# Performance work log

Hardware: AMD Instinct MI355X
Metric: run time of the kernel (lower is better)

The kernel has to match this reference:

```python
import jax, jax.numpy as jnp
import numpy as np

DIM = 512
NUM_HEADS = 16
D_HEAD = DIM // NUM_HEADS
B, S = 4, 1024


def _relative_shift(pos_score):
    # pos_score: [B, H, S1, S2] -> Transformer-XL relative shift
    b, h, s1, s2 = pos_score.shape
    padded = jnp.pad(pos_score, ((0, 0), (0, 0), (0, 0), (1, 0)))  # [B,H,S1,S2+1]
    padded = padded.reshape(b, h, s2 + 1, s1)
    return padded[:, :, 1:].reshape(b, h, s1, s2)


def setup_inputs() -> dict:
    key = jax.random.key(0)
    ks = jax.random.split(key, 16)
    f32 = jnp.float32
    scale = 0.02
    inp = {
        "query": jax.random.normal(ks[0], (B, S, DIM), f32),
        "key": jax.random.normal(ks[1], (B, S, DIM), f32),
        "value": jax.random.normal(ks[2], (B, S, DIM), f32),
        "pos_embedding": jax.random.normal(ks[3], (B, S, DIM), f32),
        "Wq": jax.random.normal(ks[4], (DIM, DIM), f32) * scale,
        "bq": jnp.zeros((DIM,), f32),
        "Wk": jax.random.normal(ks[5], (DIM, DIM), f32) * scale,
        "bk": jnp.zeros((DIM,), f32),
        "Wv": jax.random.normal(ks[6], (DIM, DIM), f32) * scale,
        "bv": jnp.zeros((DIM,), f32),
        "Wp": jax.random.normal(ks[7], (DIM, DIM), f32) * scale,  # pos_proj, no bias
        "u_bias": jax.random.normal(ks[8], (NUM_HEADS, D_HEAD), f32) * scale,
        "v_bias": jax.random.normal(ks[9], (NUM_HEADS, D_HEAD), f32) * scale,
        "Wo": jax.random.normal(ks[10], (DIM, DIM), f32) * scale,
        "bo": jnp.zeros((DIM,), f32),
    }
    return inp


def reference(query, key, value, pos_embedding, Wq, bq, Wk, bk, Wv, bv, Wp,
              u_bias, v_bias, Wo, bo):
    b = query.shape[0]
    # projections (torch Linear: x @ W.T + b), split heads -> [B, S, H, Dh]
    q = (query @ Wq.T + bq).reshape(b, -1, NUM_HEADS, D_HEAD)
    k = (key @ Wk.T + bk).reshape(b, -1, NUM_HEADS, D_HEAD)
    v = (value @ Wv.T + bv).reshape(b, -1, NUM_HEADS, D_HEAD)
    p = (pos_embedding @ Wp.T).reshape(b, -1, NUM_HEADS, D_HEAD)

    # content score: (q + u) @ k^T  -> [B, H, Sq, Sk]
    content_score = jnp.einsum('bqhd,bkhd->bhqk', q + u_bias, k)
    # position score: (q + v) @ pos^T, then relative shift
    pos_score = jnp.einsum('bqhd,bkhd->bhqk', q + v_bias, p)
    pos_score = _relative_shift(pos_score)

    score = (content_score + pos_score) / np.sqrt(D_HEAD).astype(np.float32)
    attn = jax.nn.softmax(score, axis=-1)  # dropout_p = 0.0 -> identity

    context = jnp.einsum('bhqk,bkhd->bqhd', attn, v).reshape(b, -1, DIM)
    return context @ Wo.T + bo
```

## Files before the change

kernel.cpp:

```cpp
#include <hip/hip_runtime.h>
#include <hip/hip_bf16.h>
#include <math.h>


typedef float f32x4 __attribute__((ext_vector_type(4)));
typedef __bf16 bf16x8 __attribute__((ext_vector_type(8)));
typedef __bf16 bf16x2 __attribute__((ext_vector_type(2)));

#define MFMA16(a, b, c) __builtin_amdgcn_mfma_f32_16x16x32_bf16((a), (b), (c), 0, 0, 0)

constexpr int Bb  = 4;
constexpr int S   = 1024;
constexpr int H   = 16;
constexpr int Dh  = 32;
constexpr int DIM = 512;
constexpr float SCALEL2E = 0.25501818637084186f;
constexpr int ZROWS = 3 * S + 16;

constexpr size_t XN = (size_t)Bb * S * DIM;
constexpr size_t WN = (size_t)DIM * DIM;

__device__ inline bf16x8 cvt8(const float* __restrict__ p) {
  f32x4 a = *(const f32x4*)p;
  f32x4 b = *(const f32x4*)(p + 4);
  bf16x8 r;
  r[0] = (__bf16)a[0]; r[1] = (__bf16)a[1]; r[2] = (__bf16)a[2]; r[3] = (__bf16)a[3];
  r[4] = (__bf16)b[0]; r[5] = (__bf16)b[1]; r[6] = (__bf16)b[2]; r[7] = (__bf16)b[3];
  return r;
}

__device__ inline float fexp2(float x) {
  float r;
  asm("v_exp_f32 %0, %1" : "=v"(r) : "v"(x));
  return r;
}

__device__ inline void gload_lds16(const __bf16* g, __bf16* l) {
  __builtin_amdgcn_global_load_lds(
      (const __attribute__((address_space(1))) unsigned int*)g,
      (__attribute__((address_space(3))) unsigned int*)l, 16, 0, 0);
}

__global__ __launch_bounds__(256) void conv_kernel(
    const float* __restrict__ q, const float* __restrict__ k,
    const float* __restrict__ v, const float* __restrict__ p,
    const float* __restrict__ wq, const float* __restrict__ wk,
    const float* __restrict__ wv, const float* __restrict__ wp,
    const float* __restrict__ wo,
    __bf16* __restrict__ xb, __bf16* __restrict__ wb,
    __bf16* __restrict__ phZ)
{
  const int y = blockIdx.y;
  if (y == 9) {
    const int e8 = blockIdx.x * 256 + threadIdx.x;
    if (e8 < 64 * 136 * 4) {
      const int rowIdx = e8 >> 2, chunk = e8 & 3;
      const int bh = rowIdx / 136;
      const int rl = rowIdx - bh * 136;
      const int row = (rl < 72) ? (960 + rl) : (2040 + (rl - 72));
      bf16x8 zz = {};
      *(bf16x8*)(phZ + ((size_t)bh * ZROWS + row) * Dh + chunk * 8) = zz;
    }
    return;
  }
  const float* src;
  size_t n;
  __bf16* dst;
  if (y < 4) {
    src = (y == 0) ? q : (y == 1) ? k : (y == 2) ? v : p;
    n = XN;
    dst = xb + (size_t)y * XN;
  } else {
    const int w = y - 4;
    src = (w == 0) ? wq : (w == 1) ? wk : (w == 2) ? wv : (w == 3) ? wp : wo;
    n = WN;
    dst = wb + (size_t)w * WN;
  }
  const size_t i = ((size_t)blockIdx.x * 256 + threadIdx.x) * 8;
  if (i >= n) return;
  *(bf16x8*)(dst + i) = cvt8(src + i);
}

template <int MODE>
__global__ __launch_bounds__(256) void gemm_kernel(
    const __bf16* __restrict__ xb, const __bf16* __restrict__ wb,
    const __bf16* __restrict__ ctxp,
    const float* __restrict__ bq, const float* __restrict__ bk,
    const float* __restrict__ bv, const float* __restrict__ bo,
    const float* __restrict__ ub, const float* __restrict__ vb,
    __bf16* __restrict__ qu, __bf16* __restrict__ qv,
    __bf16* __restrict__ kk, __bf16* __restrict__ vt,
    __bf16* __restrict__ phZ,
    float* __restrict__ outp)
{
  constexpr int MR = (MODE == 0) ? 4 : 2;
  constexpr int BM = MR * 32;
  __shared__ __align__(16) __bf16 smem[BM * 64 + 128 * 64];
  __bf16* As = smem;
  __bf16* Bs = smem + BM * 64;
  __bf16* trans = smem;

  const int bid = blockIdx.x;
  const int u = bid >> 3;
  const int by = u & 3;
  const int idx = (bid & 7) + 8 * (u >> 2);
  int bx, z;
  if (MODE == 0) { bx = idx & 31; z = idx >> 5; }
  else           { bx = idx;      z = 4; }

  const __bf16* Ag = (z < 4) ? (xb + (size_t)z * XN) : ctxp;
  const __bf16* Bg = wb + (size_t)z * WN;

  const int tid = threadIdx.x;
  const int wid = tid >> 6;
  const int ln = tid & 63;
  const int lm = ln & 15, lg = ln >> 4;
  const int wr = wid >> 1, wc = wid & 1;
  const int brow = bx * BM;
  const int bcol = by * 128;

  const int srow = ln >> 3;
  const int sc   = ln & 7;

  f32x4 acc[MR][4] = {};

  for (int kt = 0; kt < DIM / 64; ++kt) {
    const int k0 = kt * 64;
#pragma unroll
    for (int i = 0; i < MR; ++i) {
      const int rb = wid * (MR * 8) + i * 8;
      const int r = rb + srow;
      const int cg = sc ^ (r & 7);
      gload_lds16(Ag + (size_t)(brow + r) * DIM + k0 + cg * 8, &As[rb * 64]);
    }
#pragma unroll
    for (int i = 0; i < 4; ++i) {
      const int rb = wid * 32 + i * 8;
      const int r = rb + srow;
      const int cg = sc ^ (r & 7);
      gload_lds16(Bg + (size_t)(bcol + r) * DIM + k0 + cg * 8, &Bs[rb * 64]);
    }
    __syncthreads();

#pragma unroll
    for (int ks = 0; ks < 2; ++ks) {
      bf16x8 a[MR], b[4];
#pragma unroll
      for (int m = 0; m < MR; ++m) {
        const int row = wr * (MR * 16) + m * 16 + lm;
        const int cc = (ks * 4 + lg) ^ (row & 7);
        a[m] = *(const bf16x8*)&As[row * 64 + cc * 8];
      }
#pragma unroll
      for (int n = 0; n < 4; ++n) {
        const int row = wc * 64 + n * 16 + lm;
        const int cc = (ks * 4 + lg) ^ (row & 7);
        b[n] = *(const bf16x8*)&Bs[row * 64 + cc * 8];
      }
#pragma unroll
      for (int m = 0; m < MR; ++m)
#pragma unroll
        for (int n = 0; n < 4; ++n)
          acc[m][n] = MFMA16(a[m], b[n], acc[m][n]);
    }
    __syncthreads();
  }

  if (MODE == 0 && z == 2) {
    const int b = brow >> 10;
    const int sbase = brow & (S - 1);
#pragma unroll
    for (int n = 0; n < 4; ++n) {
      const int dl = wc * 64 + n * 16 + lm;
      const float bias = bv[bcol + dl];
#pragma unroll
      for (int mp = 0; mp < 2; ++mp) {
#pragma unroll
        for (int r = 0; r < 4; ++r) {
          const int p = wr * 64 + mp * 32 + 2 * (lg * 4 + r);
          bf16x2 pk;
          pk[0] = (__bf16)(acc[2 * mp][n][r] + bias);
          pk[1] = (__bf16)(acc[2 * mp + 1][n][r] + bias);
          const int base = dl * 128 + (((p >> 3) ^ (dl & 15)) * 8) + (p & 7);
          *(bf16x2*)(trans + base) = pk;
        }
      }
    }
    __syncthreads();
#pragma unroll
    for (int j = 0; j < 4; ++j) {
      const int dl = (tid >> 3) + j * 32;
      const int d = dl & 31, hl = dl >> 5;
      const int cp = (tid & 7) * 2;
      bf16x8 v0 = *(const bf16x8*)(trans + dl * 128 + ((cp ^ (dl & 15)) * 8));
      bf16x8 v1 = *(const bf16x8*)(trans + dl * 128 + (((cp + 1) ^ (dl & 15)) * 8));
      const int bh2 = b * H + (bcol >> 5) + hl;
      __bf16* dst = vt + ((size_t)bh2 * Dh + d) * S + sbase + cp * 8;
      *(bf16x8*)dst = v0;
      *(bf16x8*)(dst + 8) = v1;
    }
    return;
  }

#pragma unroll
  for (int n = 0; n < 4; ++n) {
    const int o = bcol + wc * 64 + n * 16 + lm;
    float bias = 0.f, ubv = 0.f, vbv = 0.f;
    if (z == 0) { bias = bq[o]; ubv = ub[o]; vbv = vb[o]; }
    else if (z == 1) bias = bk[o];
    else if (z == 4) bias = bo[o];
    const int h = o >> 5, d = o & 31;
#pragma unroll
    for (int m = 0; m < MR; ++m) {
#pragma unroll
      for (int r = 0; r < 4; ++r) {
        const int M = brow + wr * (MR * 16) + m * 16 + lg * 4 + r;
        const float val = acc[m][n][r];
        if (z == 4) {
          outp[(size_t)M * DIM + o] = val + bias;
          continue;
        }
        const int b = M >> 10, s = M & (S - 1);
        const int bh = b * H + h;
        if (z == 0) {
          const size_t idx2 = ((size_t)bh * S + s) * Dh + d;
          qu[idx2] = (__bf16)((val + bias + ubv) * SCALEL2E);
          qv[idx2] = (__bf16)((val + bias + vbv) * SCALEL2E);
        } else if (z == 1) {
          kk[((size_t)bh * S + s) * Dh + d] = (__bf16)(val + bias);
        } else {
          phZ[((size_t)bh * ZROWS + (S + 1 + s)) * Dh + d] = (__bf16)val;
        }
      }
    }
  }
}

__global__ __launch_bounds__(256, 4) void attn_kernel(
    const __bf16* __restrict__ qu, const __bf16* __restrict__ qv,
    const __bf16* __restrict__ kk, const __bf16* __restrict__ vt,
    const __bf16* __restrict__ phZ,
    __bf16* __restrict__ ctx)
{
  __shared__ __align__(16) __bf16 kv_lds[4][2][1024];
  __shared__ __align__(16) __bf16 at_all[4][2][16 * 40];

  const int tid = threadIdx.x;
  const int wid = tid >> 6;
  const int l = tid & 63;
  const int lm = l & 15, lg = l >> 4;

  const int bid = blockIdx.x;
  const int bh = (bid & 7) + 8 * ((bid >> 3) & 7);
  const int q0 = (bid >> 6) * 64 + wid * 16;
  const int h = bh & (H - 1), b = bh >> 4;

  const __bf16* qub = qu + (size_t)bh * S * Dh;
  const __bf16* qvb = qv + (size_t)bh * S * Dh;
  const __bf16* kb  = kk + (size_t)bh * S * Dh;
  const __bf16* vtb = vt + (size_t)bh * Dh * S;
  const __bf16* pZb = phZ + (size_t)bh * ZROWS * Dh;
  const __bf16* pAb = pZb + (size_t)(S + 1) * Dh;

  const bf16x8 au  = *(const bf16x8*)(qub + (size_t)(q0 + lm) * Dh + lg * 8);
  const bf16x8 avA = *(const bf16x8*)(qvb + (size_t)(q0 + lm) * Dh + lg * 8);
  const bf16x8 avB = *(const bf16x8*)(qvb + (size_t)(q0 + 1 + lm) * Dh + lg * 8);

  int  slr[4];
  bool prd[4];
#pragma unroll
  for (int r = 0; r < 4; ++r) {
    const int qr = lg * 4 + r;
    slr[r] = (l & 48) | ((lm - qr + 15) & 15);
    prd[r] = (lm <= qr);
  }

  bf16x8 ones8;
#pragma unroll
  for (int i = 0; i < 8; ++i) ones8[i] = (__bf16)1.0f;

  f32x4 cta = {0.f,0.f,0.f,0.f}, ctb = {0.f,0.f,0.f,0.f};
  f32x4 ls  = {0.f,0.f,0.f,0.f};
  const f32x4 zero4 = {0.f,0.f,0.f,0.f};

  const int srow = l >> 2;
  const int scg  = ((l & 3) ^ (srow & 3)) * 8;
  auto stage = [&](int kt, int buf) {
    const __bf16* src;
    if (wid == 0)      src = kb  + (size_t)(kt + srow) * Dh + scg;
    else if (wid == 1) src = kb  + (size_t)(kt + 16 + srow) * Dh + scg;
    else if (wid == 2) src = vtb + (size_t)srow * S + kt + scg;
    else               src = vtb + (size_t)(16 + srow) * S + kt + scg;
    gload_lds16(src, &kv_lds[buf][wid >> 1][(wid & 1) * 512]);
  };

  const int cc = (lg ^ (lm & 3)) * 8;

  auto zwin = [&](int kt, bf16x8& z0, bf16x8& z1, bf16x8& z2, bool& uB) {
    const int ktc = (kt < S) ? kt : (S - 32);
    uB = (ktc > q0 - 31);
    const int mb = ktc - q0 + (S - 16);
    const __bf16* zb = uB ? pZb : pAb;
    z0 = *(const bf16x8*)(zb + (size_t)(mb + lm) * Dh + lg * 8);
    z1 = *(const bf16x8*)(zb + (size_t)(mb + 16 + lm) * Dh + lg * 8);
    z2 = *(const bf16x8*)(zb + (size_t)(mb + 32 + lm) * Dh + lg * 8);
  };

  auto half = [&](int kt, int tb, __bf16* at,
                  bf16x8 z0, bf16x8 z1, bf16x8 z2, bool uB) {
    const __bf16* Ks = kv_lds[tb][0];
    const __bf16* Vs = kv_lds[tb][1];
    bf16x8 kf0 = *(const bf16x8*)(Ks + lm * 32 + cc);
    bf16x8 kf1 = *(const bf16x8*)(Ks + (lm + 16) * 32 + cc);
    __builtin_amdgcn_s_setprio(1);
    f32x4 c0 = MFMA16(au, kf0, zero4);
    f32x4 c1 = MFMA16(au, kf1, zero4);
    const bf16x8 av = uB ? avB : avA;
    f32x4 pt0 = MFMA16(av, z0, zero4);
    f32x4 pt1 = MFMA16(av, z1, zero4);
    f32x4 pt2 = MFMA16(av, z2, zero4);
    __builtin_amdgcn_s_setprio(0);
    if (uB && (kt < q0 + 16)) {
      const int mb = kt - q0 + (S - 16);
      bf16x8 y0 = *(const bf16x8*)(pAb + (size_t)(mb + lm) * Dh + lg * 8);
      bf16x8 y1 = *(const bf16x8*)(pAb + (size_t)(mb + 16 + lm) * Dh + lg * 8);
      bf16x8 y2 = *(const bf16x8*)(pAb + (size_t)(mb + 32 + lm) * Dh + lg * 8);
      pt0 = MFMA16(avA, y0, pt0);
      pt1 = MFMA16(avA, y1, pt1);
      pt2 = MFMA16(avA, y2, pt2);
    }

#pragma unroll
    for (int r = 0; r < 4; ++r) {
      const float v0 = __shfl(pt0[r], slr[r], 64);
      const float v1 = __shfl(pt1[r], slr[r], 64);
      const float v2 = __shfl(pt2[r], slr[r], 64);
      const float s0 = c0[r] + (prd[r] ? v0 : v1);
      const float s1 = c1[r] + (prd[r] ? v1 : v2);
      bf16x2 pp;
      pp[0] = (__bf16)fexp2(s0);
      pp[1] = (__bf16)fexp2(s1);
      *(bf16x2*)(at + (lg * 4 + r) * 40 + 2 * lm) = pp;
    }

    bf16x8 af  = *(const bf16x8*)(at + lm * 40 + lg * 8);
    bf16x8 vf0 = *(const bf16x8*)(Vs + lm * 32 + cc);
    bf16x8 vf1 = *(const bf16x8*)(Vs + (lm + 16) * 32 + cc);
    __builtin_amdgcn_s_setprio(1);
    cta = MFMA16(af, vf0, cta);
    ctb = MFMA16(af, vf1, ctb);
    ls  = MFMA16(af, ones8, ls);
    __builtin_amdgcn_s_setprio(0);
  };

  __bf16* at0 = at_all[wid][0];
  __bf16* at1 = at_all[wid][1];

  bf16x8 zA0, zA1, zA2, zB0, zB1, zB2;
  bool uA, uB;
  zwin(0, zA0, zA1, zA2, uA);
  stage(0, 0);
  stage(32, 1);
  asm volatile("s_waitcnt vmcnt(0)" ::: "memory");
  __builtin_amdgcn_s_barrier();

  for (int kt = 0; kt < S; kt += 64) {
    const int t = kt >> 5;
    stage((kt + 64 < S) ? kt + 64 : kt, (t + 2) & 3);
    stage((kt + 96 < S) ? kt + 96 : kt, (t + 3) & 3);
    zwin(kt + 32, zB0, zB1, zB2, uB);
    half(kt, t & 3, at0, zA0, zA1, zA2, uA);
    zwin(kt + 64, zA0, zA1, zA2, uA);
    half(kt + 32, (t + 1) & 3, at1, zB0, zB1, zB2, uB);

    asm volatile("s_waitcnt vmcnt(3)" ::: "memory");
    __builtin_amdgcn_s_barrier();
  }

#pragma unroll
  for (int r = 0; r < 4; ++r) {
    const int s0 = q0 + lg * 4 + r;
    const float inv = 1.f / ls[r];
    __bf16* cp = ctx + ((size_t)b * S + s0) * DIM + h * Dh;
    cp[lm]      = (__bf16)(cta[r] * inv);
    cp[16 + lm] = (__bf16)(ctb[r] * inv);
  }
}

extern "C" void kernel_launch(void* const* d_in, const int* in_sizes, int n_in,
                              void* d_out, int out_size, void* d_ws, size_t ws_size,
                              hipStream_t stream) {
  const float* query = (const float*)d_in[0];
  const float* key   = (const float*)d_in[1];
  const float* value = (const float*)d_in[2];
  const float* pos   = (const float*)d_in[3];
  const float* Wq = (const float*)d_in[4];
  const float* bq = (const float*)d_in[5];
  const float* Wk = (const float*)d_in[6];
  const float* bk = (const float*)d_in[7];
  const float* Wv = (const float*)d_in[8];
  const float* bv = (const float*)d_in[9];
  const float* Wp = (const float*)d_in[10];
  const float* ub = (const float*)d_in[11];
  const float* vb = (const float*)d_in[12];
  const float* Wo = (const float*)d_in[13];
  const float* bo = (const float*)d_in[14];
  float* out = (float*)d_out;

  char* ws = (char*)d_ws;
  const size_t MB = 1ull << 20;
  __bf16* xb  = (__bf16*)(ws + 0 * MB);
  __bf16* wb  = (__bf16*)(ws + 16 * MB);
  __bf16* qu  = (__bf16*)(ws + 19 * MB);
  __bf16* qv  = (__bf16*)(ws + 23 * MB);
  __bf16* kk  = (__bf16*)(ws + 27 * MB);
  __bf16* vt  = (__bf16*)(ws + 31 * MB);
  __bf16* phZ = (__bf16*)(ws + 35 * MB);
  __bf16* ctx = (__bf16*)(ws + 48 * MB);

  conv_kernel<<<dim3(1024, 10), dim3(256), 0, stream>>>(
      query, key, value, pos, Wq, Wk, Wv, Wp, Wo, xb, wb, phZ);

  gemm_kernel<0><<<dim3(512), dim3(256), 0, stream>>>(
      xb, wb, ctx, bq, bk, bv, bo, ub, vb,
      qu, qv, kk, vt, phZ, out);

  attn_kernel<<<dim3(1024), dim3(256), 0, stream>>>(
      qu, qv, kk, vt, phZ, ctx);

  gemm_kernel<1><<<dim3(256), dim3(256), 0, stream>>>(
      xb, wb, ctx, bq, bk, bv, bo, ub, vb,
      qu, qv, kk, vt, phZ, out);
}
```

Baseline: 84.21 us.

## Reuse overlapping positional windows across tiles and change LDS swizzle pattern

The positional window loads for consecutive 32-key tiles overlap by 16 rows, so the third chunk of one window is reused as the first chunk of the next when both come from the same buffer. This removes one global/L2 load per half-tile in the common case. The K/V LDS swizzle is also changed to XOR with a different row-bit group, on both the staging writes and the fragment reads, to alter the bank conflict pattern. There is a risk that the extra branches and the register dependencies across halves lengthen live ranges or serialize loads.

```diff
diff --git a/kernel.cpp b/kernel.cpp
--- a/kernel.cpp
+++ b/kernel.cpp
@@ -284,7 +284,7 @@
   const f32x4 zero4 = {0.f,0.f,0.f,0.f};
 
   const int srow = l >> 2;
-  const int scg  = ((l & 3) ^ (srow & 3)) * 8;
+  const int scg  = ((l & 3) ^ ((l >> 3) & 3)) * 8;
   auto stage = [&](int kt, int buf) {
     const __bf16* src;
     if (wid == 0)      src = kb  + (size_t)(kt + srow) * Dh + scg;
@@ -294,20 +294,16 @@
     gload_lds16(src, &kv_lds[buf][wid >> 1][(wid & 1) * 512]);
   };
 
-  const int cc = (lg ^ (lm & 3)) * 8;
-
-  auto zwin = [&](int kt, bf16x8& z0, bf16x8& z1, bf16x8& z2, bool& uB) {
-    const int ktc = (kt < S) ? kt : (S - 32);
-    uB = (ktc > q0 - 31);
+  const int cc = (lg ^ ((lm >> 1) & 3)) * 8;
+
+  auto zld = [&](int ktc, int off, bool uB_) -> bf16x8 {
     const int mb = ktc - q0 + (S - 16);
-    const __bf16* zb = uB ? pZb : pAb;
-    z0 = *(const bf16x8*)(zb + (size_t)(mb + lm) * Dh + lg * 8);
-    z1 = *(const bf16x8*)(zb + (size_t)(mb + 16 + lm) * Dh + lg * 8);
-    z2 = *(const bf16x8*)(zb + (size_t)(mb + 32 + lm) * Dh + lg * 8);
+    const __bf16* zb = uB_ ? pZb : pAb;
+    return *(const bf16x8*)(zb + (size_t)(mb + off + lm) * Dh + lg * 8);
   };
 
   auto half = [&](int kt, int tb, __bf16* at,
-                  bf16x8 z0, bf16x8 z1, bf16x8 z2, bool uB) {
+                  bf16x8 z0, bf16x8 z1, bf16x8 z2, bool uB_) {
     const __bf16* Ks = kv_lds[tb][0];
     const __bf16* Vs = kv_lds[tb][1];
     bf16x8 kf0 = *(const bf16x8*)(Ks + lm * 32 + cc);
@@ -315,12 +311,12 @@
     __builtin_amdgcn_s_setprio(1);
     f32x4 c0 = MFMA16(au, kf0, zero4);
     f32x4 c1 = MFMA16(au, kf1, zero4);
-    const bf16x8 av = uB ? avB : avA;
+    const bf16x8 av = uB_ ? avB : avA;
     f32x4 pt0 = MFMA16(av, z0, zero4);
     f32x4 pt1 = MFMA16(av, z1, zero4);
     f32x4 pt2 = MFMA16(av, z2, zero4);
     __builtin_amdgcn_s_setprio(0);
-    if (uB && (kt < q0 + 16)) {
+    if (uB_ && (kt < q0 + 16)) {
       const int mb = kt - q0 + (S - 16);
       bf16x8 y0 = *(const bf16x8*)(pAb + (size_t)(mb + lm) * Dh + lg * 8);
       bf16x8 y1 = *(const bf16x8*)(pAb + (size_t)(mb + 16 + lm) * Dh + lg * 8);
@@ -356,9 +352,11 @@
   __bf16* at0 = at_all[wid][0];
   __bf16* at1 = at_all[wid][1];
 
-  bf16x8 zA0, zA1, zA2, zB0, zB1, zB2;
-  bool uA, uB;
-  zwin(0, zA0, zA1, zA2, uA);
+  bf16x8 zA0, zA1, zA2;
+  bool uA = (0 > q0 - 31);
+  zA0 = zld(0, 0, uA);
+  zA1 = zld(0, 16, uA);
+  zA2 = zld(0, 32, uA);
   stage(0, 0);
   stage(32, 1);
   asm volatile("s_waitcnt vmcnt(0)" ::: "memory");
@@ -368,10 +366,26 @@
     const int t = kt >> 5;
     stage((kt + 64 < S) ? kt + 64 : kt, (t + 2) & 3);
     stage((kt + 96 < S) ? kt + 96 : kt, (t + 3) & 3);
-    zwin(kt + 32, zB0, zB1, zB2, uB);
+
+    const bool uB = ((kt + 32) > q0 - 31);
+    bf16x8 zB0;
+    if (uB == uA) zB0 = zA2;
+    else          zB0 = zld(kt + 32, 0, uB);
+    bf16x8 zB1 = zld(kt + 32, 16, uB);
+    bf16x8 zB2 = zld(kt + 32, 32, uB);
+
     half(kt, t & 3, at0, zA0, zA1, zA2, uA);
-    zwin(kt + 64, zA0, zA1, zA2, uA);
+
+    const int ktn = (kt + 64 < S) ? kt + 64 : (S - 32);
+    const bool uAn = (ktn > q0 - 31);
+    zA1 = zld(ktn, 16, uAn);
+    zA2 = zld(ktn, 32, uAn);
+
     half(kt + 32, (t + 1) & 3, at1, zB0, zB1, zB2, uB);
+
+    if (uAn == uB) zA0 = zB2;
+    else           zA0 = zld(ktn, 0, uAn);
+    uA = uAn;
 
     asm volatile("s_waitcnt vmcnt(3)" ::: "memory");
     __builtin_amdgcn_s_barrier();
```

New measurement: 82.80 us. Within noise of the previous version (-1.7%).
